# Kernel tuning notes

Measured on AMD Instinct MI355X. Metric: run time of the kernel, lower is better.

Reference implementation:

```python
import jax, jax.numpy as jnp
import numpy as np

B, S, D = 2, 1024, 1024
E = 8          # routed experts
I = 1024       # per-expert intermediate
IS = 1024      # shared expert intermediate
TOP_K = 2
NUM_SHARED = 1


def setup_inputs() -> dict:
    key = jax.random.key(0)
    ks = jax.random.split(key, 8)
    scale = 0.02
    return {
        "x": jax.random.normal(ks[0], (B, S, D), dtype=jnp.float32),
        "w_gate": jax.random.normal(ks[1], (D, E), dtype=jnp.float32) * scale,
        "wg": jax.random.normal(ks[2], (E, D, I), dtype=jnp.float32) * scale,  # expert gate_proj
        "wu": jax.random.normal(ks[3], (E, D, I), dtype=jnp.float32) * scale,  # expert up_proj
        "wd": jax.random.normal(ks[4], (E, I, D), dtype=jnp.float32) * scale,  # expert down_proj
        "ws_g": jax.random.normal(ks[5], (NUM_SHARED, D, IS), dtype=jnp.float32) * scale,
        "ws_u": jax.random.normal(ks[6], (NUM_SHARED, D, IS), dtype=jnp.float32) * scale,
        "ws_d": jax.random.normal(ks[7], (NUM_SHARED, IS, D), dtype=jnp.float32) * scale,
    }


def _swiglu(t, w_gate_proj, w_up, w_down):
    # t: [N, D]
    g = t @ w_gate_proj            # [N, I]
    u = t @ w_up                   # [N, I]
    return (jax.nn.silu(g) * u) @ w_down  # [N, D]


def reference(x, w_gate, wg, wu, wd, ws_g, ws_u, ws_d):
    Bb, Ss, Dd = x.shape
    x_flat = x.reshape(Bb * Ss, Dd)                  # [N, D]
    N = x_flat.shape[0]

    # --- router ---
    logits = x_flat @ w_gate                          # [N, E]
    topk_logits, topk_idx = jax.lax.top_k(logits, TOP_K)
    topk_w = jax.nn.softmax(topk_logits, axis=-1)     # [N, K]

    # --- aux load-balancing loss ---
    one_hot = jax.nn.one_hot(topk_idx, E, dtype=jnp.float32)  # [N, K, E]
    f = one_hot.sum(axis=1).mean(axis=0)                       # [E]
    P = jax.nn.softmax(logits, axis=-1).mean(axis=0)           # [E]
    aux_loss = E * jnp.sum(f * P)

    # --- combine weights: cw[n, e] = sum_k topk_w[n,k] * 1[topk_idx[n,k]==e] ---
    cw = jnp.einsum("nk,nke->ne", topk_w, one_hot)             # [N, E]

    # --- routed experts: dense compute over all experts, weighted combine ---
    g = jnp.einsum("nd,edi->eni", x_flat, wg)                  # [E, N, I]
    u = jnp.einsum("nd,edi->eni", x_flat, wu)                  # [E, N, I]
    a = jax.nn.silu(g) * u                                     # [E, N, I]
    y = jnp.einsum("eni,eid->end", a, wd)                      # [E, N, D]
    routed = jnp.einsum("ne,end->nd", cw, y)                   # [N, D]

    # --- shared experts ---
    shared = jnp.zeros_like(x_flat)
    for s in range(NUM_SHARED):
        shared = shared + _swiglu(x_flat, ws_g[s], ws_u[s], ws_d[s])

    out = (routed + shared).reshape(Bb, Ss, Dd)
    return out, aux_loss
```

## Files before the change

kernel.cpp:

```cpp
#include <hip/hip_runtime.h>
#include <math.h>

typedef unsigned short u16;
typedef __attribute__((ext_vector_type(8))) short short8;
typedef __attribute__((ext_vector_type(4))) float f32x4;
typedef __attribute__((ext_vector_type(4))) unsigned short u16x4;
typedef __attribute__((ext_vector_type(8))) unsigned short u16x8;

#define N_TOK 2048
#define DIM 1024
#define OUT_ELEMS 2097152

#define GLDS16(gp, lp) __builtin_amdgcn_global_load_lds( \
    (const __attribute__((address_space(1))) unsigned int*)(gp), \
    (__attribute__((address_space(3))) unsigned int*)(lp), 16, 0, 0)

__device__ __forceinline__ u16 f2bf(float f) {
    union { float f; unsigned u; } v; v.f = f;
    unsigned r = (v.u + 0x7FFFu + ((v.u >> 16) & 1u)) >> 16;
    return (u16)r;
}
__device__ __forceinline__ float bf2f(u16 h) {
    union { unsigned u; float f; } v; v.u = ((unsigned)h) << 16;
    return v.f;
}

__device__ __forceinline__ void cvt_chunk(const float* __restrict__ src,
                                          u16* __restrict__ dst, int chunk,
                                          char* smem, int t) {
    float* tile = (float*)smem;
    const char* gsrc = (const char*)(src + (size_t)chunk * 8192);
    u16* dchunk = dst + (size_t)chunk * 8192;
    int w = t >> 6, l = t & 63;
#pragma unroll
    for (int j = 0; j < 8; j++) {
        int idx = w * 8 + j;
        GLDS16(gsrc + idx * 1024 + l * 16, smem + idx * 1024);
    }
    __syncthreads();
    int n0 = (t & 63) * 4 + (t >> 6) * 256;
    f32x4 v[8];
#pragma unroll
    for (int k = 0; k < 8; k++)
        v[k] = *(const f32x4*)(tile + k * 1024 + n0);
#pragma unroll
    for (int i = 0; i < 4; i++) {
        u16x8 o;
#pragma unroll
        for (int k = 0; k < 8; k++) o[k] = f2bf(v[k][i]);
        *(u16x8*)(dchunk + (size_t)(n0 + i) * 8) = o;
    }
}

__device__ __forceinline__ void cvt_chunk512(const float* __restrict__ src,
                                             u16* __restrict__ dst, int chunk,
                                             char* smem, int t) {
    float* tile = (float*)smem;
    const char* gsrc = (const char*)(src + (size_t)chunk * 8192);
    u16* dchunk = dst + (size_t)chunk * 8192;
    int w = t >> 6, l = t & 63;
#pragma unroll
    for (int j = 0; j < 4; j++) {
        int idx = w * 4 + j;
        GLDS16(gsrc + idx * 1024 + l * 16, smem + idx * 1024);
    }
    __syncthreads();
    int n0 = (t & 63) * 2 + (t >> 6) * 128;
    float2 v[8];
#pragma unroll
    for (int k = 0; k < 8; k++)
        v[k] = *(const float2*)(tile + k * 1024 + n0);
#pragma unroll
    for (int i = 0; i < 2; i++) {
        u16x8 o;
#pragma unroll
        for (int k = 0; k < 8; k++) o[k] = f2bf(i ? v[k].y : v[k].x);
        *(u16x8*)(dchunk + (size_t)(n0 + i) * 8) = o;
    }
}

__device__ __forceinline__ void cvt_gu_job(int j, const float* wg, const float* wu,
                                           const float* wsg, const float* wsu,
                                           u16* wgt, u16* wut, u16* wsgt, u16* wsut,
                                           char* smem, int t) {
    int mat = j >> 7, chunk = j & 127;
    const float* src; u16* dst;
    if      (mat <  8) { src = wg + (size_t)mat * 1048576;       dst = wgt + (size_t)mat * 1048576; }
    else if (mat < 16) { src = wu + (size_t)(mat - 8) * 1048576; dst = wut + (size_t)(mat - 8) * 1048576; }
    else if (mat == 16){ src = wsg; dst = wsgt; }
    else               { src = wsu; dst = wsut; }
    cvt_chunk(src, dst, chunk, smem, t);
}

__device__ __forceinline__ void cvt_d_job512(int j, const float* wd, const float* wsd,
                                             u16* wdt, u16* wsdt, char* smem, int t) {
    int mat = j >> 7, chunk = j & 127;
    const float* src = (mat < 8) ? (wd + (size_t)mat * 1048576) : wsd;
    u16* dst = (mat < 8) ? (wdt + (size_t)mat * 1048576) : wsdt;
    cvt_chunk512(src, dst, chunk, smem, t);
}

__device__ __forceinline__ void router_job(int b, const float* x, const float* wgate,
                                           u16* xb, int* tidx, float* tw,
                                           float* Pp, int* Cp, int* tlist,
                                           int* curs, char* smem, int t) {
    float* sP = (float*)smem;
    int*   sC = (int*)(smem + 64);
    if (t < 8) { sP[t] = 0.f; sC[t] = 0; }
    if (b == 0 && t < 16) curs[t] = 0;
    __syncthreads();
    int wave = t >> 6;
    int lane = t & 63;
    int n = b * 4 + wave;
    const float* xr = x + (size_t)n * DIM;
    u16* xbr = xb + (size_t)n * DIM;
    float acc[8] = {0.f,0.f,0.f,0.f,0.f,0.f,0.f,0.f};
#pragma unroll
    for (int i = 0; i < 16; i++) {
        int d = lane + i * 64;
        float xv = xr[d];
        xbr[d] = f2bf(xv);
        const float* wr = wgate + d * 8;
#pragma unroll
        for (int e = 0; e < 8; e++) acc[e] += xv * wr[e];
    }
#pragma unroll
    for (int off = 32; off; off >>= 1) {
#pragma unroll
        for (int e = 0; e < 8; e++) acc[e] += __shfl_xor(acc[e], off);
    }
    if (lane == 0) {
        tlist[4096 + n] = n;
        float mx = acc[0];
#pragma unroll
        for (int e = 1; e < 8; e++) mx = fmaxf(mx, acc[e]);
        float p[8], s = 0.f;
#pragma unroll
        for (int e = 0; e < 8; e++) { p[e] = expf(acc[e] - mx); s += p[e]; }
        float inv = 1.f / s;
#pragma unroll
        for (int e = 0; e < 8; e++) atomicAdd(&sP[e], p[e] * inv);
        int i0 = 0; float b0 = acc[0];
#pragma unroll
        for (int e = 1; e < 8; e++) if (acc[e] > b0) { b0 = acc[e]; i0 = e; }
        int i1 = -1; float b1 = -3.4e38f;
#pragma unroll
        for (int e = 0; e < 8; e++) if (e != i0 && acc[e] > b1) { b1 = acc[e]; i1 = e; }
        float w0 = 1.f / (1.f + expf(b1 - b0));
        tidx[n * 2] = i0; tidx[n * 2 + 1] = i1;
        tw[n * 2] = w0;   tw[n * 2 + 1] = 1.f - w0;
        atomicAdd(&sC[i0], 1);
        atomicAdd(&sC[i1], 1);
    }
    __syncthreads();
    if (t < 8) { Pp[b * 8 + t] = sP[t]; Cp[b * 8 + t] = sC[t]; }
}

__device__ __forceinline__ void scatter_job(int bid, const int* tidx, const float* Pp,
                                            const int* Cp, int* curs, int* tlist,
                                            int* slots, float* out, int* counts,
                                            int* offs, char* smem, int t) {
    int*   s_off = (int*)smem;
    int*   sCnt  = (int*)(smem + 32);
    float* sPs   = (float*)(smem + 64);
    int*   redC  = (int*)(smem + 128);
    float* redP  = (float*)(smem + 1152);
    int e = t & 7, g = t >> 3;
    int cs = 0; float ps = 0.f;
#pragma unroll
    for (int j = 0; j < 16; j++) {
        int b = g + j * 32;
        cs += Cp[b * 8 + e];
        ps += Pp[b * 8 + e];
    }
    redC[t] = cs; redP[t] = ps;
    __syncthreads();
    if (t < 8) {
        int c = 0; float p = 0.f;
        for (int g2 = 0; g2 < 32; g2++) { c += redC[g2 * 8 + t]; p += redP[g2 * 8 + t]; }
        sCnt[t] = c; sPs[t] = p;
    }
    __syncthreads();
    if (t == 0) {
        int o = 0;
        for (int e2 = 0; e2 < 8; e2++) { s_off[e2] = o; o += sCnt[e2]; }
    }
    __syncthreads();
    if (bid == 0 && t == 0) {
        float aux = 0.f;
        for (int e2 = 0; e2 < 8; e2++) {
            aux += (float)sCnt[e2] * sPs[e2];
            offs[e2] = s_off[e2]; counts[e2] = sCnt[e2];
        }
        out[OUT_ELEMS] = 8.f * aux / ((float)N_TOK * (float)N_TOK);
        offs[8] = 4096; counts[8] = 2048;
    }
    int n = bid * 256 + t;
    if (n < N_TOK) {
#pragma unroll
        for (int k = 0; k < 2; k++) {
            int ee = tidx[n * 2 + k];
            int p = atomicAdd(&curs[ee], 1);
            int sl = s_off[ee] + p;
            tlist[sl] = n;
            slots[n * 2 + k] = sl;
        }
    }
}

__device__ __forceinline__ void gemm_map(int jj, int& job, int& mt, int& nt) {
    if (jj < 128) { job = 8; mt = jj >> 3; nt = jj & 7; }
    else {
        int r = jj - 128;
        mt = r >> 6;
        int rem = r & 63;
        job = rem >> 3;
        nt = rem & 7;
    }
}

__device__ __forceinline__ void gemm1_job(
    int jj, const u16* __restrict__ xb, const u16* __restrict__ wgt,
    const u16* __restrict__ wut, const u16* __restrict__ wsgt,
    const u16* __restrict__ wsut, const int* __restrict__ tlist,
    const int* __restrict__ counts, const int* __restrict__ offs,
    u16* __restrict__ H, char* smem, int t) {
    int job, mt, nt; gemm_map(jj, job, mt, nt);
    int jcnt = counts[job];
    int m0 = mt << 7;
    if (m0 >= jcnt) return;
    int joff = offs[job];
    int n0 = nt << 7;
    const u16* Bg = (job < 8) ? (wgt + (size_t)job * 1048576) : wsgt;
    const u16* Bu = (job < 8) ? (wut + (size_t)job * 1048576) : wsut;

    int wave = t >> 6, lane = t & 63;
    int arow = wave * 16 + (lane >> 2);
    int tok = tlist[joff + m0 + arow];
    const u16* aA = xb + (size_t)tok * 1024 + (lane & 3) * 8;
    int cwv = wave & 3;
    const u16* pB = ((wave < 4) ? Bg : Bu) + (size_t)cwv * 8192
                  + (size_t)(n0 + lane) * 8;
    int bOff = ((wave < 4) ? 8192 : 16384) + cwv * 2048;

    int wm = (wave >> 1) << 5;
    int wn = (wave & 1) << 6;
    int quad = lane >> 4, lr = lane & 15;

    f32x4 accg[2][4], accu[2][4];
    f32x4 zz = {0.f, 0.f, 0.f, 0.f};
#pragma unroll
    for (int i = 0; i < 2; i++)
#pragma unroll
        for (int j = 0; j < 4; j++) { accg[i][j] = zz; accu[i][j] = zz; }

#define STAGE1(b_, s_) do { \
        char* bb = smem + (b_) * 24576; \
        int k0_ = (s_) * 32; \
        size_t koff_ = (size_t)k0_ * 1024; \
        GLDS16(aA + k0_, (u16*)bb + wave * 512); \
        GLDS16(pB + koff_,       (u16*)(bb + bOff)); \
        GLDS16(pB + koff_ + 512, (u16*)(bb + bOff + 1024)); \
    } while (0)

    STAGE1(0, 0);
    __syncthreads();
    for (int s = 0; s < 32; s++) {
        int cur = s & 1;
        if (s < 31) STAGE1(cur ^ 1, s + 1);
        const char* cb = smem + cur * 24576;
        const u16* Asr = (const u16*)cb;
        const u16* Bgr = (const u16*)(cb + 8192);
        const u16* Bur = (const u16*)(cb + 16384);
        short8 af[2], bgf[4], buf[4];
#pragma unroll
        for (int i = 0; i < 2; i++)
            af[i] = *(const short8*)(Asr + (wm + i * 16 + lr) * 32 + quad * 8);
#pragma unroll
        for (int i = 0; i < 4; i++) {
            int nrow = wn + i * 16 + lr;
            bgf[i] = *(const short8*)(Bgr + quad * 1024 + nrow * 8);
            buf[i] = *(const short8*)(Bur + quad * 1024 + nrow * 8);
        }
#pragma unroll
        for (int mi = 0; mi < 2; mi++)
#pragma unroll
            for (int ni = 0; ni < 4; ni++) {
                accg[mi][ni] = __builtin_amdgcn_mfma_f32_16x16x32_bf16(af[mi], bgf[ni], accg[mi][ni], 0, 0, 0);
                accu[mi][ni] = __builtin_amdgcn_mfma_f32_16x16x32_bf16(af[mi], buf[ni], accu[mi][ni], 0, 0, 0);
            }
        __syncthreads();
    }
#undef STAGE1
#pragma unroll
    for (int mi = 0; mi < 2; mi++) {
        int rowb = m0 + wm + mi * 16 + quad * 4;
#pragma unroll
        for (int rr = 0; rr < 4; rr++) {
            int row = rowb + rr;
            if (row < jcnt) {
                size_t base = (size_t)(joff + row) * 1024 + n0 + wn;
#pragma unroll
                for (int ni = 0; ni < 4; ni++) {
                    float g = accg[mi][ni][rr];
                    float u = accu[mi][ni][rr];
                    float h = (g / (1.f + expf(-g))) * u;
                    H[base + ni * 16 + lr] = f2bf(h);
                }
            }
        }
    }
}

__device__ __forceinline__ void gemm2_job(
    int jj, const u16* __restrict__ H, const u16* __restrict__ wdt,
    const u16* __restrict__ wsdt, const int* __restrict__ counts,
    const int* __restrict__ offs, u16* __restrict__ Y, char* smem, int t) {
    int job, mt, nt; gemm_map(jj, job, mt, nt);
    int jcnt = counts[job];
    int m0 = mt << 7;
    if (m0 >= jcnt) return;
    int joff = offs[job];
    int n0 = nt << 7;
    const u16* Bt = (job < 8) ? (wdt + (size_t)job * 1048576) : wsdt;

    int wave = t >> 6, lane = t & 63;
    int arow = wave * 16 + (lane >> 2);
    const u16* aA = H + (size_t)(joff + m0 + arow) * 1024 + (lane & 3) * 8;
    int cwv = wave >> 1, half = wave & 1;
    const u16* pB = Bt + (size_t)cwv * 8192 + (size_t)(n0 + half * 64 + lane) * 8;
    int bOff = 8192 + cwv * 2048 + half * 1024;

    int wm = (wave >> 1) << 5;
    int wn = (wave & 1) << 6;
    int quad = lane >> 4, lr = lane & 15;

    f32x4 acc[2][4];
    f32x4 zz = {0.f, 0.f, 0.f, 0.f};
#pragma unroll
    for (int i = 0; i < 2; i++)
#pragma unroll
        for (int j = 0; j < 4; j++) acc[i][j] = zz;

#define STAGE2(b_, s_) do { \
        char* bb = smem + (b_) * 16384; \
        int k0_ = (s_) * 32; \
        size_t koff_ = (size_t)k0_ * 1024; \
        GLDS16(aA + k0_, (u16*)bb + wave * 512); \
        GLDS16(pB + koff_, (u16*)(bb + bOff)); \
    } while (0)

    STAGE2(0, 0);
    __syncthreads();
    for (int s = 0; s < 32; s++) {
        int cur = s & 1;
        if (s < 31) STAGE2(cur ^ 1, s + 1);
        const char* cb = smem + cur * 16384;
        const u16* Asr = (const u16*)cb;
        const u16* Bsr = (const u16*)(cb + 8192);
        short8 af[2], bf[4];
#pragma unroll
        for (int i = 0; i < 2; i++)
            af[i] = *(const short8*)(Asr + (wm + i * 16 + lr) * 32 + quad * 8);
#pragma unroll
        for (int i = 0; i < 4; i++)
            bf[i] = *(const short8*)(Bsr + quad * 1024 + (wn + i * 16 + lr) * 8);
#pragma unroll
        for (int mi = 0; mi < 2; mi++)
#pragma unroll
            for (int ni = 0; ni < 4; ni++)
                acc[mi][ni] = __builtin_amdgcn_mfma_f32_16x16x32_bf16(af[mi], bf[ni], acc[mi][ni], 0, 0, 0);
        __syncthreads();
    }
#undef STAGE2
#pragma unroll
    for (int mi = 0; mi < 2; mi++) {
        int rowb = m0 + wm + mi * 16 + quad * 4;
#pragma unroll
        for (int rr = 0; rr < 4; rr++) {
            int row = rowb + rr;
            if (row < jcnt) {
                u16* yrow = Y + (size_t)(joff + row) * 1024 + n0 + wn;
#pragma unroll
                for (int ni = 0; ni < 4; ni++)
                    yrow[ni * 16 + lr] = f2bf(acc[mi][ni][rr]);
            }
        }
    }
}

__device__ __forceinline__ void combine_job(int n, const u16* __restrict__ Y,
                                            const int* __restrict__ slots,
                                            const float* __restrict__ tw,
                                            float* __restrict__ out, int t) {
    int s0 = slots[n * 2], s1 = slots[n * 2 + 1];
    float w0 = tw[n * 2], w1 = tw[n * 2 + 1];
    u16x4 y0 = ((const u16x4*)(Y + (size_t)s0 * 1024))[t];
    u16x4 y1 = ((const u16x4*)(Y + (size_t)s1 * 1024))[t];
    u16x4 ys = ((const u16x4*)(Y + (size_t)(4096 + n) * 1024))[t];
    f32x4 r;
    r.x = w0 * bf2f(y0.x) + w1 * bf2f(y1.x) + bf2f(ys.x);
    r.y = w0 * bf2f(y0.y) + w1 * bf2f(y1.y) + bf2f(ys.y);
    r.z = w0 * bf2f(y0.z) + w1 * bf2f(y1.z) + bf2f(ys.z);
    r.w = w0 * bf2f(y0.w) + w1 * bf2f(y1.w) + bf2f(ys.w);
    ((f32x4*)(out + (size_t)n * 1024))[t] = r;
}

__global__ __launch_bounds__(256)
void k_front(const float* __restrict__ wg, const float* __restrict__ wu,
             const float* __restrict__ wsg, const float* __restrict__ wsu,
             u16* __restrict__ wgt, u16* __restrict__ wut,
             u16* __restrict__ wsgt, u16* __restrict__ wsut,
             const float* __restrict__ x, const float* __restrict__ wgate,
             u16* __restrict__ xb, int* __restrict__ tidx, float* __restrict__ tw,
             float* __restrict__ Pp, int* __restrict__ Cp,
             int* __restrict__ tlist, int* __restrict__ curs) {
    __shared__ __attribute__((aligned(128))) char smem[32768];
    int bx = blockIdx.x, t = threadIdx.x;
    if (bx < 512) router_job(bx, x, wgate, xb, tidx, tw, Pp, Cp, tlist, curs, smem, t);
    else          cvt_gu_job(bx - 512, wg, wu, wsg, wsu, wgt, wut, wsgt, wsut, smem, t);
}

__global__ void k_scatter(const int* __restrict__ tidx, const float* __restrict__ Pp,
                          const int* __restrict__ Cp, int* __restrict__ curs,
                          int* __restrict__ tlist, int* __restrict__ slots,
                          float* __restrict__ out, int* __restrict__ counts,
                          int* __restrict__ offs) {
    __shared__ __attribute__((aligned(128))) char smem[4096];
    scatter_job(blockIdx.x, tidx, Pp, Cp, curs, tlist, slots, out, counts, offs,
                smem, threadIdx.x);
}

__global__ __launch_bounds__(512, 2)
void k_gemm1(const u16* __restrict__ xb, const u16* __restrict__ wgt,
             const u16* __restrict__ wut, const u16* __restrict__ wsgt,
             const u16* __restrict__ wsut, const int* __restrict__ tlist,
             const int* __restrict__ counts, const int* __restrict__ offs,
             u16* __restrict__ H,
             const float* __restrict__ wd, const float* __restrict__ wsd,
             u16* __restrict__ wdt, u16* __restrict__ wsdt) {
    __shared__ __attribute__((aligned(128))) char smem[49152];
    int bx = blockIdx.x, t = threadIdx.x;
    if (bx < 1152) gemm1_job(bx, xb, wgt, wut, wsgt, wsut, tlist, counts, offs, H, smem, t);
    else           cvt_d_job512(bx - 1152, wd, wsd, wdt, wsdt, smem, t);
}

__global__ __launch_bounds__(512, 2)
void k_gemm2(const u16* __restrict__ H, const u16* __restrict__ wdt,
             const u16* __restrict__ wsdt, const int* __restrict__ counts,
             const int* __restrict__ offs, u16* __restrict__ Y) {
    __shared__ __attribute__((aligned(128))) char smem[32768];
    gemm2_job(blockIdx.x, H, wdt, wsdt, counts, offs, Y, smem, threadIdx.x);
}

__global__ void k_combine(const u16* __restrict__ Y, const int* __restrict__ slots,
                          const float* __restrict__ tw, float* __restrict__ out) {
    combine_job(blockIdx.x, Y, slots, tw, out, threadIdx.x);
}

extern "C" void kernel_launch(void* const* d_in, const int* in_sizes, int n_in,
                              void* d_out, int out_size, void* d_ws, size_t ws_size,
                              hipStream_t stream) {
    const float* x     = (const float*)d_in[0];
    const float* wgate = (const float*)d_in[1];
    const float* wg    = (const float*)d_in[2];
    const float* wu    = (const float*)d_in[3];
    const float* wd    = (const float*)d_in[4];
    const float* wsg   = (const float*)d_in[5];
    const float* wsu   = (const float*)d_in[6];
    const float* wsd   = (const float*)d_in[7];
    float* out = (float*)d_out;

    char* ws = (char*)d_ws;
    u16*   xb    = (u16*)(ws + 0);
    u16*   wgt   = (u16*)(ws + 4194304);
    u16*   wut   = (u16*)(ws + 20971520);
    u16*   wdt   = (u16*)(ws + 37748736);
    u16*   wsgt  = (u16*)(ws + 54525952);
    u16*   wsut  = (u16*)(ws + 56623104);
    u16*   wsdt  = (u16*)(ws + 58720256);
    u16*   H     = (u16*)(ws + 60817408);
    u16*   Y     = (u16*)(ws + 4194304);
    int*   tidx  = (int*)(ws + 73400320);
    float* tw    = (float*)(ws + 73416704);
    int*   tlist = (int*)(ws + 73433088);
    int*   slots = (int*)(ws + 73457664);
    int*   counts= (int*)(ws + 73474048);
    int*   offs  = (int*)(ws + 73474112);
    int*   curs  = (int*)(ws + 73474176);
    float* Pp    = (float*)(ws + 73474304);
    int*   Cp    = (int*)(ws + 73490688);

    k_front<<<2816, 256, 0, stream>>>(wg, wu, wsg, wsu, wgt, wut, wsgt, wsut,
                                      x, wgate, xb, tidx, tw, Pp, Cp, tlist, curs);
    k_scatter<<<8, 256, 0, stream>>>(tidx, Pp, Cp, curs, tlist, slots,
                                     out, counts, offs);
    k_gemm1<<<2304, 512, 0, stream>>>(xb, wgt, wut, wsgt, wsut, tlist, counts, offs,
                                      H, wd, wsd, wdt, wsdt);
    k_gemm2<<<1152, 512, 0, stream>>>(H, wdt, wsdt, counts, offs, Y);
    k_combine<<<2048, 256, 0, stream>>>(Y, slots, tw, out);
}
```

Baseline: 235.8 us.

## Triple-buffer LDS in both expert GEMMs with vmcnt-based waits

Both grouped GEMM main loops move from double-buffered LDS staging to a three-stage ring, with loads issued two K-steps ahead. The single __syncthreads per step becomes an s_waitcnt vmcnt(N) plus s_barrier, so the newest prefetch can stay in flight while the barrier is crossed. The goal is to hide global-to-LDS latency behind MFMA work. In exchange, LDS use rises to 72KB and 48KB per block, which may lower occupancy under launch_bounds(512,2) on the 160KB LDS.

```diff
diff --git a/kernel.cpp b/kernel.cpp
--- a/kernel.cpp
+++ b/kernel.cpp
@@ -14,6 +14,13 @@
 #define GLDS16(gp, lp) __builtin_amdgcn_global_load_lds( \
     (const __attribute__((address_space(1))) unsigned int*)(gp), \
     (__attribute__((address_space(3))) unsigned int*)(lp), 16, 0, 0)
+
+#define WAITV_N(n) do { \
+    asm volatile("s_waitcnt vmcnt(" #n ")" ::: "memory"); \
+    __builtin_amdgcn_sched_barrier(0); \
+    __builtin_amdgcn_s_barrier(); \
+    __builtin_amdgcn_sched_barrier(0); \
+} while (0)
 
 __device__ __forceinline__ u16 f2bf(float f) {
     union { float f; unsigned u; } v; v.f = f;
@@ -264,10 +271,14 @@
     } while (0)
 
     STAGE1(0, 0);
-    __syncthreads();
+    STAGE1(1, 1);
+    WAITV_N(3);
+    int cur = 0;
     for (int s = 0; s < 32; s++) {
-        int cur = s & 1;
-        if (s < 31) STAGE1(cur ^ 1, s + 1);
+        if (s < 30) {
+            int nb = cur + 2; if (nb >= 3) nb -= 3;
+            STAGE1(nb, s + 2);
+        }
         const char* cb = smem + cur * 24576;
         const u16* Asr = (const u16*)cb;
         const u16* Bgr = (const u16*)(cb + 8192);
@@ -289,7 +300,11 @@
                 accg[mi][ni] = __builtin_amdgcn_mfma_f32_16x16x32_bf16(af[mi], bgf[ni], accg[mi][ni], 0, 0, 0);
                 accu[mi][ni] = __builtin_amdgcn_mfma_f32_16x16x32_bf16(af[mi], buf[ni], accu[mi][ni], 0, 0, 0);
             }
-        __syncthreads();
+        if (s < 31) {
+            if (s < 30) WAITV_N(3);
+            else        WAITV_N(0);
+        }
+        cur = cur + 1; if (cur >= 3) cur -= 3;
     }
 #undef STAGE1
 #pragma unroll
@@ -351,10 +366,14 @@
     } while (0)
 
     STAGE2(0, 0);
-    __syncthreads();
+    STAGE2(1, 1);
+    WAITV_N(2);
+    int cur = 0;
     for (int s = 0; s < 32; s++) {
-        int cur = s & 1;
-        if (s < 31) STAGE2(cur ^ 1, s + 1);
+        if (s < 30) {
+            int nb = cur + 2; if (nb >= 3) nb -= 3;
+            STAGE2(nb, s + 2);
+        }
         const char* cb = smem + cur * 16384;
         const u16* Asr = (const u16*)cb;
         const u16* Bsr = (const u16*)(cb + 8192);
@@ -370,7 +389,11 @@
 #pragma unroll
             for (int ni = 0; ni < 4; ni++)
                 acc[mi][ni] = __builtin_amdgcn_mfma_f32_16x16x32_bf16(af[mi], bf[ni], acc[mi][ni], 0, 0, 0);
-        __syncthreads();
+        if (s < 31) {
+            if (s < 30) WAITV_N(2);
+            else        WAITV_N(0);
+        }
+        cur = cur + 1; if (cur >= 3) cur -= 3;
     }
 #undef STAGE2
 #pragma unroll
@@ -439,7 +462,7 @@
              u16* __restrict__ H,
              const float* __restrict__ wd, const float* __restrict__ wsd,
              u16* __restrict__ wdt, u16* __restrict__ wsdt) {
-    __shared__ __attribute__((aligned(128))) char smem[49152];
+    __shared__ __attribute__((aligned(128))) char smem[73728];
     int bx = blockIdx.x, t = threadIdx.x;
     if (bx < 1152) gemm1_job(bx, xb, wgt, wut, wsgt, wsut, tlist, counts, offs, H, smem, t);
     else           cvt_d_job512(bx - 1152, wd, wsd, wdt, wsdt, smem, t);
@@ -449,7 +472,7 @@
 void k_gemm2(const u16* __restrict__ H, const u16* __restrict__ wdt,
              const u16* __restrict__ wsdt, const int* __restrict__ counts,
              const int* __restrict__ offs, u16* __restrict__ Y) {
-    __shared__ __attribute__((aligned(128))) char smem[32768];
+    __shared__ __attribute__((aligned(128))) char smem[49152];
     gemm2_job(blockIdx.x, H, wdt, wsdt, counts, offs, Y, smem, threadIdx.x);
 }
 
```

Measured after the change: 231.4 us. Within noise of the previous version (-1.8%).

## Split router from weight conversion and interleave gemm1 with down-proj conversion

Applied to the files above, without the earlier changes.

Splits the fused front kernel into a small router kernel with a reduced LDS footprint and a separate gate/up weight conversion kernel, launched after the scatter. In gemm1, blocks now alternate between GEMM tiles and down-proj conversion jobs instead of running all conversions at the end. GEMM tile order in gemm1 and gemm2 is permuted with a multiplicative stride to spread expert/tile work across CUs. This trades one extra kernel launch for better co-scheduling of memory-bound conversion work with compute-bound GEMM and better load balance across uneven expert tiles.

```diff
diff --git a/kernel.cpp b/kernel.cpp
--- a/kernel.cpp
+++ b/kernel.cpp
@@ -407,18 +407,23 @@
 }
 
 __global__ __launch_bounds__(256)
-void k_front(const float* __restrict__ wg, const float* __restrict__ wu,
-             const float* __restrict__ wsg, const float* __restrict__ wsu,
-             u16* __restrict__ wgt, u16* __restrict__ wut,
-             u16* __restrict__ wsgt, u16* __restrict__ wsut,
-             const float* __restrict__ x, const float* __restrict__ wgate,
-             u16* __restrict__ xb, int* __restrict__ tidx, float* __restrict__ tw,
-             float* __restrict__ Pp, int* __restrict__ Cp,
-             int* __restrict__ tlist, int* __restrict__ curs) {
+void k_router(const float* __restrict__ x, const float* __restrict__ wgate,
+              u16* __restrict__ xb, int* __restrict__ tidx, float* __restrict__ tw,
+              float* __restrict__ Pp, int* __restrict__ Cp,
+              int* __restrict__ tlist, int* __restrict__ curs) {
+    __shared__ __attribute__((aligned(128))) char smem[4096];
+    router_job(blockIdx.x, x, wgate, xb, tidx, tw, Pp, Cp, tlist, curs,
+               smem, threadIdx.x);
+}
+
+__global__ __launch_bounds__(256)
+void k_cvt(const float* __restrict__ wg, const float* __restrict__ wu,
+           const float* __restrict__ wsg, const float* __restrict__ wsu,
+           u16* __restrict__ wgt, u16* __restrict__ wut,
+           u16* __restrict__ wsgt, u16* __restrict__ wsut) {
     __shared__ __attribute__((aligned(128))) char smem[32768];
-    int bx = blockIdx.x, t = threadIdx.x;
-    if (bx < 512) router_job(bx, x, wgate, xb, tidx, tw, Pp, Cp, tlist, curs, smem, t);
-    else          cvt_gu_job(bx - 512, wg, wu, wsg, wsu, wgt, wut, wsgt, wsut, smem, t);
+    cvt_gu_job(blockIdx.x, wg, wu, wsg, wsu, wgt, wut, wsgt, wsut,
+               smem, threadIdx.x);
 }
 
 __global__ void k_scatter(const int* __restrict__ tidx, const float* __restrict__ Pp,
@@ -441,8 +446,12 @@
              u16* __restrict__ wdt, u16* __restrict__ wsdt) {
     __shared__ __attribute__((aligned(128))) char smem[49152];
     int bx = blockIdx.x, t = threadIdx.x;
-    if (bx < 1152) gemm1_job(bx, xb, wgt, wut, wsgt, wsut, tlist, counts, offs, H, smem, t);
-    else           cvt_d_job512(bx - 1152, wd, wsd, wdt, wsdt, smem, t);
+    if (bx & 1) {
+        cvt_d_job512(bx >> 1, wd, wsd, wdt, wsdt, smem, t);
+    } else {
+        int jj = ((bx >> 1) * 577) % 1152;
+        gemm1_job(jj, xb, wgt, wut, wsgt, wsut, tlist, counts, offs, H, smem, t);
+    }
 }
 
 __global__ __launch_bounds__(512, 2)
@@ -450,7 +459,8 @@
              const u16* __restrict__ wsdt, const int* __restrict__ counts,
              const int* __restrict__ offs, u16* __restrict__ Y) {
     __shared__ __attribute__((aligned(128))) char smem[32768];
-    gemm2_job(blockIdx.x, H, wdt, wsdt, counts, offs, Y, smem, threadIdx.x);
+    int jj = (blockIdx.x * 577) % 1152;
+    gemm2_job(jj, H, wdt, wsdt, counts, offs, Y, smem, threadIdx.x);
 }
 
 __global__ void k_combine(const u16* __restrict__ Y, const int* __restrict__ slots,
@@ -491,10 +501,10 @@
     float* Pp    = (float*)(ws + 73474304);
     int*   Cp    = (int*)(ws + 73490688);
 
-    k_front<<<2816, 256, 0, stream>>>(wg, wu, wsg, wsu, wgt, wut, wsgt, wsut,
-                                      x, wgate, xb, tidx, tw, Pp, Cp, tlist, curs);
+    k_router<<<512, 256, 0, stream>>>(x, wgate, xb, tidx, tw, Pp, Cp, tlist, curs);
     k_scatter<<<8, 256, 0, stream>>>(tidx, Pp, Cp, curs, tlist, slots,
                                      out, counts, offs);
+    k_cvt<<<2304, 256, 0, stream>>>(wg, wu, wsg, wsu, wgt, wut, wsgt, wsut);
     k_gemm1<<<2304, 512, 0, stream>>>(xb, wgt, wut, wsgt, wsut, tlist, counts, offs,
                                       H, wd, wsd, wdt, wsdt);
     k_gemm2<<<1152, 512, 0, stream>>>(H, wdt, wsdt, counts, offs, Y);
```

Measured after the change: 274.3 us. +16.3%, slower.

## Replace static GEMM grids with persistent blocks pulling compact job queue

Applied to the files above, without the earlier changes.

The scatter kernel now builds a compact list of only the non-empty GEMM tiles (shared expert first, then each routed expert up to its token count), ordered by N-tile then M-tile. The GEMM kernels launch 512 persistent blocks that pull jobs from that list with an atomic counter. gemm1 then continues on to the down-weight conversion jobs. This avoids launching and early-exiting the empty tiles of the dense grid and improves load balance. In exchange it adds an atomic and two barriers per job, serial job-list construction by one thread, and a changed tile order that affects cache reuse.

```diff
diff --git a/kernel.cpp b/kernel.cpp
--- a/kernel.cpp
+++ b/kernel.cpp
@@ -156,76 +156,12 @@
     if (t < 8) { Pp[b * 8 + t] = sP[t]; Cp[b * 8 + t] = sC[t]; }
 }
 
-__device__ __forceinline__ void scatter_job(int bid, const int* tidx, const float* Pp,
-                                            const int* Cp, int* curs, int* tlist,
-                                            int* slots, float* out, int* counts,
-                                            int* offs, char* smem, int t) {
-    int*   s_off = (int*)smem;
-    int*   sCnt  = (int*)(smem + 32);
-    float* sPs   = (float*)(smem + 64);
-    int*   redC  = (int*)(smem + 128);
-    float* redP  = (float*)(smem + 1152);
-    int e = t & 7, g = t >> 3;
-    int cs = 0; float ps = 0.f;
-#pragma unroll
-    for (int j = 0; j < 16; j++) {
-        int b = g + j * 32;
-        cs += Cp[b * 8 + e];
-        ps += Pp[b * 8 + e];
-    }
-    redC[t] = cs; redP[t] = ps;
-    __syncthreads();
-    if (t < 8) {
-        int c = 0; float p = 0.f;
-        for (int g2 = 0; g2 < 32; g2++) { c += redC[g2 * 8 + t]; p += redP[g2 * 8 + t]; }
-        sCnt[t] = c; sPs[t] = p;
-    }
-    __syncthreads();
-    if (t == 0) {
-        int o = 0;
-        for (int e2 = 0; e2 < 8; e2++) { s_off[e2] = o; o += sCnt[e2]; }
-    }
-    __syncthreads();
-    if (bid == 0 && t == 0) {
-        float aux = 0.f;
-        for (int e2 = 0; e2 < 8; e2++) {
-            aux += (float)sCnt[e2] * sPs[e2];
-            offs[e2] = s_off[e2]; counts[e2] = sCnt[e2];
-        }
-        out[OUT_ELEMS] = 8.f * aux / ((float)N_TOK * (float)N_TOK);
-        offs[8] = 4096; counts[8] = 2048;
-    }
-    int n = bid * 256 + t;
-    if (n < N_TOK) {
-#pragma unroll
-        for (int k = 0; k < 2; k++) {
-            int ee = tidx[n * 2 + k];
-            int p = atomicAdd(&curs[ee], 1);
-            int sl = s_off[ee] + p;
-            tlist[sl] = n;
-            slots[n * 2 + k] = sl;
-        }
-    }
-}
-
-__device__ __forceinline__ void gemm_map(int jj, int& job, int& mt, int& nt) {
-    if (jj < 128) { job = 8; mt = jj >> 3; nt = jj & 7; }
-    else {
-        int r = jj - 128;
-        mt = r >> 6;
-        int rem = r & 63;
-        job = rem >> 3;
-        nt = rem & 7;
-    }
-}
-
 __device__ __forceinline__ void gemm1_job(
-    int jj, const u16* __restrict__ xb, const u16* __restrict__ wgt,
-    const u16* __restrict__ wut, const u16* __restrict__ wsgt,
-    const u16* __restrict__ wsut, const int* __restrict__ tlist,
-    const int* __restrict__ counts, const int* __restrict__ offs,
-    u16* __restrict__ H, char* smem, int t) {
-    int job, mt, nt; gemm_map(jj, job, mt, nt);
+    int job, int mt, int nt, const u16* __restrict__ xb,
+    const u16* __restrict__ wgt, const u16* __restrict__ wut,
+    const u16* __restrict__ wsgt, const u16* __restrict__ wsut,
+    const int* __restrict__ tlist, const int* __restrict__ counts,
+    const int* __restrict__ offs, u16* __restrict__ H, char* smem, int t) {
     int jcnt = counts[job];
     int m0 = mt << 7;
     if (m0 >= jcnt) return;
@@ -313,10 +249,10 @@
 }
 
 __device__ __forceinline__ void gemm2_job(
-    int jj, const u16* __restrict__ H, const u16* __restrict__ wdt,
-    const u16* __restrict__ wsdt, const int* __restrict__ counts,
-    const int* __restrict__ offs, u16* __restrict__ Y, char* smem, int t) {
-    int job, mt, nt; gemm_map(jj, job, mt, nt);
+    int job, int mt, int nt, const u16* __restrict__ H,
+    const u16* __restrict__ wdt, const u16* __restrict__ wsdt,
+    const int* __restrict__ counts, const int* __restrict__ offs,
+    u16* __restrict__ Y, char* smem, int t) {
     int jcnt = counts[job];
     int m0 = mt << 7;
     if (m0 >= jcnt) return;
@@ -425,10 +361,70 @@
                           const int* __restrict__ Cp, int* __restrict__ curs,
                           int* __restrict__ tlist, int* __restrict__ slots,
                           float* __restrict__ out, int* __restrict__ counts,
-                          int* __restrict__ offs) {
-    __shared__ __attribute__((aligned(128))) char smem[4096];
-    scatter_job(blockIdx.x, tidx, Pp, Cp, curs, tlist, slots, out, counts, offs,
-                smem, threadIdx.x);
+                          int* __restrict__ offs, int* __restrict__ jobs,
+                          int* __restrict__ njobs, int* __restrict__ qh1,
+                          int* __restrict__ qh2) {
+    __shared__ int   s_off[8];
+    __shared__ int   sCnt[8];
+    __shared__ float sPs[8];
+    __shared__ int   redC[256];
+    __shared__ float redP[256];
+    int bid = blockIdx.x;
+    int t = threadIdx.x;
+    int e = t & 7, g = t >> 3;
+    int cs = 0; float ps = 0.f;
+#pragma unroll
+    for (int j = 0; j < 16; j++) {
+        int b = g + j * 32;
+        cs += Cp[b * 8 + e];
+        ps += Pp[b * 8 + e];
+    }
+    redC[t] = cs; redP[t] = ps;
+    __syncthreads();
+    if (t < 8) {
+        int c = 0; float p = 0.f;
+        for (int g2 = 0; g2 < 32; g2++) { c += redC[g2 * 8 + t]; p += redP[g2 * 8 + t]; }
+        sCnt[t] = c; sPs[t] = p;
+    }
+    __syncthreads();
+    if (t == 0) {
+        int o = 0;
+        for (int e2 = 0; e2 < 8; e2++) { s_off[e2] = o; o += sCnt[e2]; }
+    }
+    __syncthreads();
+    if (bid == 0 && t == 0) {
+        float aux = 0.f;
+        for (int e2 = 0; e2 < 8; e2++) {
+            aux += (float)sCnt[e2] * sPs[e2];
+            offs[e2] = s_off[e2]; counts[e2] = sCnt[e2];
+        }
+        out[OUT_ELEMS] = 8.f * aux / ((float)N_TOK * (float)N_TOK);
+        offs[8] = 4096; counts[8] = 2048;
+        int nj = 0;
+        for (int nt2 = 0; nt2 < 8; nt2++)
+            for (int mt2 = 0; mt2 < 16; mt2++)
+                jobs[nj++] = (8 << 8) | (mt2 << 3) | nt2;
+        for (int e2 = 0; e2 < 8; e2++) {
+            int mtm = (sCnt[e2] + 127) >> 7;
+            if (mtm > 16) mtm = 16;
+            for (int nt2 = 0; nt2 < 8; nt2++)
+                for (int mt2 = 0; mt2 < mtm; mt2++)
+                    jobs[nj++] = (e2 << 8) | (mt2 << 3) | nt2;
+        }
+        *njobs = nj;
+        *qh1 = 0; *qh2 = 0;
+    }
+    int n = bid * 256 + t;
+    if (n < N_TOK) {
+#pragma unroll
+        for (int k = 0; k < 2; k++) {
+            int ee = tidx[n * 2 + k];
+            int p = atomicAdd(&curs[ee], 1);
+            int sl = s_off[ee] + p;
+            tlist[sl] = n;
+            slots[n * 2 + k] = sl;
+        }
+    }
 }
 
 __global__ __launch_bounds__(512, 2)
@@ -438,19 +434,49 @@
              const int* __restrict__ counts, const int* __restrict__ offs,
              u16* __restrict__ H,
              const float* __restrict__ wd, const float* __restrict__ wsd,
-             u16* __restrict__ wdt, u16* __restrict__ wsdt) {
+             u16* __restrict__ wdt, u16* __restrict__ wsdt,
+             const int* __restrict__ jobs, const int* __restrict__ njobs,
+             int* __restrict__ qh) {
     __shared__ __attribute__((aligned(128))) char smem[49152];
-    int bx = blockIdx.x, t = threadIdx.x;
-    if (bx < 1152) gemm1_job(bx, xb, wgt, wut, wsgt, wsut, tlist, counts, offs, H, smem, t);
-    else           cvt_d_job512(bx - 1152, wd, wsd, wdt, wsdt, smem, t);
+    __shared__ int sj;
+    int t = threadIdx.x;
+    int nj = *njobs;
+    for (;;) {
+        if (t == 0) sj = atomicAdd(qh, 1);
+        __syncthreads();
+        int j = sj;
+        __syncthreads();
+        if (j >= nj + 1152) break;
+        if (j < nj) {
+            int p = jobs[j];
+            gemm1_job(p >> 8, (p >> 3) & 31, p & 7, xb, wgt, wut, wsgt, wsut,
+                      tlist, counts, offs, H, smem, t);
+        } else {
+            cvt_d_job512(j - nj, wd, wsd, wdt, wsdt, smem, t);
+        }
+    }
 }
 
 __global__ __launch_bounds__(512, 2)
 void k_gemm2(const u16* __restrict__ H, const u16* __restrict__ wdt,
              const u16* __restrict__ wsdt, const int* __restrict__ counts,
-             const int* __restrict__ offs, u16* __restrict__ Y) {
+             const int* __restrict__ offs, u16* __restrict__ Y,
+             const int* __restrict__ jobs, const int* __restrict__ njobs,
+             int* __restrict__ qh) {
     __shared__ __attribute__((aligned(128))) char smem[32768];
-    gemm2_job(blockIdx.x, H, wdt, wsdt, counts, offs, Y, smem, threadIdx.x);
+    __shared__ int sj;
+    int t = threadIdx.x;
+    int nj = *njobs;
+    for (;;) {
+        if (t == 0) sj = atomicAdd(qh, 1);
+        __syncthreads();
+        int j = sj;
+        __syncthreads();
+        if (j >= nj) break;
+        int p = jobs[j];
+        gemm2_job(p >> 8, (p >> 3) & 31, p & 7, H, wdt, wsdt, counts, offs,
+                  Y, smem, t);
+    }
 }
 
 __global__ void k_combine(const u16* __restrict__ Y, const int* __restrict__ slots,
@@ -490,13 +516,18 @@
     int*   curs  = (int*)(ws + 73474176);
     float* Pp    = (float*)(ws + 73474304);
     int*   Cp    = (int*)(ws + 73490688);
+    int*   jobs  = (int*)(ws + 73507072);
+    int*   njobs = (int*)(ws + 73516288);
+    int*   qh1   = (int*)(ws + 73516292);
+    int*   qh2   = (int*)(ws + 73516296);
 
     k_front<<<2816, 256, 0, stream>>>(wg, wu, wsg, wsu, wgt, wut, wsgt, wsut,
                                       x, wgate, xb, tidx, tw, Pp, Cp, tlist, curs);
     k_scatter<<<8, 256, 0, stream>>>(tidx, Pp, Cp, curs, tlist, slots,
-                                     out, counts, offs);
-    k_gemm1<<<2304, 512, 0, stream>>>(xb, wgt, wut, wsgt, wsut, tlist, counts, offs,
-                                      H, wd, wsd, wdt, wsdt);
-    k_gemm2<<<1152, 512, 0, stream>>>(H, wdt, wsdt, counts, offs, Y);
+                                     out, counts, offs, jobs, njobs, qh1, qh2);
+    k_gemm1<<<512, 512, 0, stream>>>(xb, wgt, wut, wsgt, wsut, tlist, counts, offs,
+                                     H, wd, wsd, wdt, wsdt, jobs, njobs, qh1);
+    k_gemm2<<<512, 512, 0, stream>>>(H, wdt, wsdt, counts, offs, Y,
+                                     jobs, njobs, qh2);
     k_combine<<<2048, 256, 0, stream>>>(Y, slots, tw, out);
 }
```

Result: slower. 269.8 us (+14.4%).
